# Kernel optimization log

Measured on AMD Instinct MI355X. Metric: run time of the kernel, lower is better.

Reference implementation:

```python
import jax, jax.numpy as jnp
import numpy as np

B, MN, GN, ME, GE = 1, 40962, 65160, 327660, 163848
MEMB = EEMB = 256
H1, H2 = 512, 64
EPS = 1e-5


def setup_inputs() -> dict:
    key = jax.random.key(0)
    ks = jax.random.split(key, 16)
    s = 0.05
    return {
        "gx": jax.random.normal(ks[0], (B, GN, MEMB), jnp.float32),
        "mx": jax.random.normal(ks[1], (B, MN, MEMB), jnp.float32),
        "me_i": jax.random.randint(ks[2], (2, ME), 0, MN),
        "me_x": jax.random.normal(ks[3], (B, ME, EEMB), jnp.float32),
        "g2me_i": jax.random.randint(ks[4], (2, GE), 0, MN),
        "g2me_x": jax.random.normal(ks[5], (B, GE, EEMB), jnp.float32),
        "m2ge_i": jax.random.randint(ks[6], (2, GE), 0, MN),
        "m2ge_x": jax.random.normal(ks[7], (B, GE, EEMB), jnp.float32),
        # learned params (Linear stored as [in, out]; y = x @ W + b, math-equivalent to torch)
        "W1": jax.random.normal(ks[8], (2 * MEMB + EEMB, H1), jnp.float32) * s,
        "b1": jnp.zeros((H1,), jnp.float32),
        "W2": jax.random.normal(ks[9], (H1, H2), jnp.float32) * s,
        "b2": jnp.zeros((H2,), jnp.float32),
        "W3": jax.random.normal(ks[10], (H2, EEMB), jnp.float32) * s,
        "b3": jnp.zeros((EEMB,), jnp.float32),
        # LayerNorm([m_enum, eemb]) -> elementwise affine over last two dims
        "ln_w": jnp.ones((ME, EEMB), jnp.float32),
        "ln_b": jnp.zeros((ME, EEMB), jnp.float32),
    }


def reference(gx, mx, me_i, me_x, g2me_i, g2me_x, m2ge_i, m2ge_x,
              W1, b1, W2, b2, W3, b3, ln_w, ln_b):
    row, col = me_i[0], me_i[1]
    # gather sender/receiver mesh-node features per edge: [B, ME, 2*MEMB+EEMB]
    h = jnp.concatenate([mx[:, row], mx[:, col], me_x], axis=-1)
    h = jax.nn.silu(h @ W1 + b1)
    h = jax.nn.silu(h @ W2 + b2)
    h = h @ W3 + b3
    # LayerNorm over the last TWO dims (m_enum, eemb), as nn.LayerNorm([m_enum, eemb])
    mean = jnp.mean(h, axis=(-2, -1), keepdims=True)
    var = jnp.var(h, axis=(-2, -1), keepdims=True)
    h = (h - mean) * jax.lax.rsqrt(var + EPS) * ln_w + ln_b
    me_x_new = me_x + h
    return (gx, mx, me_i, me_x_new, g2me_i, g2me_x, m2ge_i, m2ge_x)
```

## Files before the change

kernel.cpp:

```cpp
#include <hip/hip_runtime.h>
#include <hip/hip_bf16.h>

typedef unsigned short u16;
typedef unsigned int u32;
typedef __attribute__((ext_vector_type(8))) short bfrag8;
typedef __attribute__((ext_vector_type(4))) float f32x4;

#define ME_N 327660
#define MN_N 40962
#define MEMB_N 256
#define H1_N 512
#define H2_N 64
#define EEMB_N 256
#define LN_EPS 1e-5f
#define NBLK 5120

static __device__ __forceinline__ u16 f2bf(float f) {
  __hip_bfloat16 h = __float2bfloat16(f);
  return *reinterpret_cast<u16*>(&h);
}
static __device__ __forceinline__ float bf2f(u16 u) {
  union { u32 i; float f; } x; x.i = ((u32)u) << 16; return x.f;
}
static __device__ __forceinline__ u32 pack2(float a, float b) {
  return (u32)f2bf(a) | ((u32)f2bf(b) << 16);
}
static __device__ __forceinline__ float silu_f(float x) {
  return x / (1.0f + __expf(-x));
}
static __device__ __forceinline__ void gload_lds16(const void* g, void* l) {
  __builtin_amdgcn_global_load_lds(
      (const __attribute__((address_space(1))) void*)g,
      (__attribute__((address_space(3))) void*)l, 16, 0, 0);
}

__global__ void i2f_kernel(const int* __restrict__ src, float* __restrict__ dst, int n) {
  int i = blockIdx.x * 256 + threadIdx.x;
  if (i < n) dst[i] = (float)src[i];
}

__global__ void bfconv_kernel(const float* __restrict__ src, u16* __restrict__ dst, int n) {
  int i = (blockIdx.x * 256 + threadIdx.x) * 8;
  if (i >= n) return;
  float4 v0 = reinterpret_cast<const float4*>(src + i)[0];
  float4 v1 = reinterpret_cast<const float4*>(src + i)[1];
  uint4 q;
  q.x = pack2(v0.x, v0.y); q.y = pack2(v0.z, v0.w);
  q.z = pack2(v1.x, v1.y); q.w = pack2(v1.z, v1.w);
  *reinterpret_cast<uint4*>(dst + i) = q;
}

__global__ void wconv1_kernel(const float* __restrict__ src, u16* __restrict__ dst) {
  int i = blockIdx.x * 256 + threadIdx.x;
  if (i >= 512 * 768) return;
  int e   = i & 7;
  int l16 = (i >> 3) & 15;
  int k4  = (i >> 7) & 3;
  int ks  = (i >> 9) & 1;
  int rest = i >> 10;
  int kc = rest % 12;
  int J  = rest / 12;
  int n = J * 16 + l16;
  int k = kc * 64 + ks * 32 + k4 * 8 + e;
  dst[i] = f2bf(src[(size_t)k * 512 + n]);
}

__global__ void wconv_kernel(const float* __restrict__ src, u16* __restrict__ dst,
                             int K, int N) {
  int i = blockIdx.x * 256 + threadIdx.x;
  if (i >= K * N) return;
  int n = i / K;
  int k = i - n * K;
  dst[i] = f2bf(src[(size_t)k * N + n]);
}

__launch_bounds__(1024, 4)
__global__ void gemm_fused_kernel(const u16* __restrict__ mxb, const int* __restrict__ me_i,
                                  const float* __restrict__ me_x,
                                  const u16* __restrict__ w1f, const float* __restrict__ b1,
                                  const u16* __restrict__ w2t, const float* __restrict__ b2,
                                  const u16* __restrict__ w3t, const float* __restrict__ b3,
                                  u16* __restrict__ h3, float* __restrict__ partials) {
  __shared__ u16 S[16384];
  __shared__ float red[32];

  const int t = threadIdx.x;
  const int m0 = blockIdx.x * 64;
  const int lane = t & 63;
  const int w = t >> 6;
  const int l16 = lane & 15;
  const int k4 = lane >> 4;
  const int h7 = l16 & 7;

  const int r_st = (t >> 3) & 63;
  const int g_st = t & 7;
  const int gsw = (g_st ^ (r_st & 7)) * 8;
  const int mg = min(m0 + r_st, ME_N - 1);
  const u16* rowr = mxb + (size_t)me_i[mg] * MEMB_N;
  const u16* rowc = mxb + (size_t)me_i[ME_N + mg] * MEMB_N;

  const int r4 = t >> 4;
  const int sub = t & 15;
  const int sgrp = sub >> 1, shalf = sub & 1;
  const int mg4 = min(m0 + r4, ME_N - 1);
  const float* pef = me_x + (size_t)mg4 * EEMB_N + ((sgrp ^ (r4 & 7)) * 8 + shalf * 4);
  const int doff = r4 * 64 + sgrp * 8 + shalf * 4;

  const f32x4 zero = {0.f, 0.f, 0.f, 0.f};
  f32x4 acc[2][4];
#pragma unroll
  for (int jj = 0; jj < 2; ++jj)
#pragma unroll
    for (int i = 0; i < 4; ++i) acc[jj][i] = zero;

  auto stage_dma = [&](int kcn) {
    if (w < 8) {
      const u16* src = (kcn < 4 ? rowr : rowc) + (kcn & 3) * 64 + gsw;
      gload_lds16(src, S + (kcn & 3) * 4096 + w * 512);
    }
  };
  auto loadB = [&](int kc, bfrag8 (&bfr)[2][2]) {
    const u16* wbase = w1f + (size_t)(w * 2) * 12288 + (size_t)kc * 1024 + k4 * 128 + l16 * 8;
#pragma unroll
    for (int ks = 0; ks < 2; ++ks)
#pragma unroll
      for (int jj = 0; jj < 2; ++jj)
        bfr[ks][jj] = *reinterpret_cast<const bfrag8*>(wbase + (size_t)jj * 12288 + ks * 512);
  };
  auto compute = [&](int kc, const bfrag8 (&bfr)[2][2]) {
    const u16* ab = S + (kc & 3) * 4096;
#pragma unroll
    for (int ks = 0; ks < 2; ++ks) {
      bfrag8 a[4];
#pragma unroll
      for (int i = 0; i < 4; ++i)
        a[i] = *reinterpret_cast<const bfrag8*>(
            &ab[(i * 16 + l16) * 64 + (((ks * 4 + k4) ^ h7) * 8)]);
#pragma unroll
      for (int jj = 0; jj < 2; ++jj)
#pragma unroll
        for (int i = 0; i < 4; ++i)
          acc[jj][i] = __builtin_amdgcn_mfma_f32_16x16x32_bf16(bfr[ks][jj], a[i], acc[jj][i], 0, 0, 0);
    }
  };
  auto packA = [&](const float4& fq, int slot) {
    uint2 pq = make_uint2(pack2(fq.x, fq.y), pack2(fq.z, fq.w));
    *reinterpret_cast<uint2*>(S + slot * 4096 + doff) = pq;
  };

#define WAITDMA() if (w < 8) { asm volatile("s_waitcnt vmcnt(10)" ::: "memory"); }
#define BAR() __builtin_amdgcn_s_barrier(); asm volatile("" ::: "memory")
#define LGKM0() asm volatile("s_waitcnt lgkmcnt(0)" ::: "memory")

  bfrag8 B0[2][2], B1[2][2];
  float4 fqA, fqB, fqC, fqD;

  stage_dma(0);
  asm volatile("s_waitcnt vmcnt(63)" ::: "memory");
  stage_dma(1);
  asm volatile("s_waitcnt vmcnt(63)" ::: "memory");
  stage_dma(2);
  loadB(0, B0);

  loadB(1, B1); WAITDMA(); BAR(); stage_dma(3); compute(0, B0);
  loadB(2, B0); WAITDMA(); BAR(); stage_dma(4); compute(1, B1);
  loadB(3, B1); WAITDMA(); BAR(); stage_dma(5); compute(2, B0);
  loadB(4, B0); WAITDMA(); BAR(); stage_dma(6); compute(3, B1);
  loadB(5, B1); WAITDMA(); BAR(); stage_dma(7); compute(4, B0);
  loadB(6, B0); WAITDMA(); BAR();
  fqA = *reinterpret_cast<const float4*>(pef);
  compute(5, B1);
  loadB(7, B1); WAITDMA(); BAR();
  fqB = *reinterpret_cast<const float4*>(pef + 64);
  compute(6, B0);
  loadB(8, B0); WAITDMA(); BAR();
  fqC = *reinterpret_cast<const float4*>(pef + 128);
  compute(7, B1);
  packA(fqA, 0); LGKM0();
  loadB(9, B1); BAR();
  fqD = *reinterpret_cast<const float4*>(pef + 192);
  compute(8, B0);
  packA(fqB, 1); LGKM0();
  loadB(10, B0); BAR();
  compute(9, B1);
  packA(fqC, 2); LGKM0();
  loadB(11, B1); BAR();
  compute(10, B0);
  packA(fqD, 3); LGKM0();
  BAR();
  compute(11, B1);

#undef WAITDMA
#undef BAR
#undef LGKM0

  __syncthreads();

  const int kh = w >> 3;
  const int n2s = w & 3;
  const int ihalf = (w >> 2) & 1;
  const int n2 = n2s * 16 + l16;

  f32x4 acc2p[2];
#pragma unroll
  for (int ii = 0; ii < 2; ++ii) acc2p[ii] = zero;

#pragma unroll
  for (int h = 0; h < 2; ++h) {
    if (kh == h) {
#pragma unroll
      for (int jj = 0; jj < 2; ++jj) {
        const int colbase = (w & 7) * 32 + jj * 16 + k4 * 4;
        const float4 bq = *reinterpret_cast<const float4*>(b1 + h * 256 + colbase);
        const int grp = colbase >> 3, off = colbase & 7;
#pragma unroll
        for (int i = 0; i < 4; ++i) {
          float x0 = silu_f(acc[jj][i][0] + bq.x);
          float x1 = silu_f(acc[jj][i][1] + bq.y);
          float x2 = silu_f(acc[jj][i][2] + bq.z);
          float x3 = silu_f(acc[jj][i][3] + bq.w);
          uint2 pq = make_uint2(pack2(x0, x1), pack2(x2, x3));
          *reinterpret_cast<uint2*>(&S[(i * 16 + l16) * 256 + ((grp ^ h7) * 8 + off)]) = pq;
        }
      }
    }
    __syncthreads();
    if (kh == h) {
#pragma unroll
      for (int ksl = 0; ksl < 8; ++ksl) {
        bfrag8 w2f = *reinterpret_cast<const bfrag8*>(
            w2t + (size_t)n2 * 512 + h * 256 + ksl * 32 + k4 * 8);
#pragma unroll
        for (int ii = 0; ii < 2; ++ii) {
          const int i = ihalf * 2 + ii;
          bfrag8 a2 = *reinterpret_cast<const bfrag8*>(
              &S[(i * 16 + l16) * 256 + (((ksl * 4 + k4) ^ h7) * 8)]);
          acc2p[ii] = __builtin_amdgcn_mfma_f32_16x16x32_bf16(w2f, a2, acc2p[ii], 0, 0, 0);
        }
      }
    }
    __syncthreads();
  }

  float* LDSf = reinterpret_cast<float*>(S);
  u16* h2T = S + 12288;
  if (kh == 1) {
#pragma unroll
    for (int ii = 0; ii < 2; ++ii)
      *reinterpret_cast<f32x4*>(
          &LDSf[(((n2s * 2 + ihalf) * 2 + ii) * 64 + lane) * 4]) = acc2p[ii];
  }
  __syncthreads();
  if (kh == 0) {
    const float4 b2q = *reinterpret_cast<const float4*>(b2 + n2s * 16 + k4 * 4);
    const int grpn = n2s * 2 + (k4 >> 1), offn = (k4 & 1) * 4;
#pragma unroll
    for (int ii = 0; ii < 2; ++ii) {
      const int i = ihalf * 2 + ii;
      f32x4 o = *reinterpret_cast<f32x4*>(
          &LDSf[(((n2s * 2 + ihalf) * 2 + ii) * 64 + lane) * 4]);
      float x0 = silu_f(acc2p[ii][0] + o[0] + b2q.x);
      float x1 = silu_f(acc2p[ii][1] + o[1] + b2q.y);
      float x2 = silu_f(acc2p[ii][2] + o[2] + b2q.z);
      float x3 = silu_f(acc2p[ii][3] + o[3] + b2q.w);
      uint2 pq = make_uint2(pack2(x0, x1), pack2(x2, x3));
      *reinterpret_cast<uint2*>(&h2T[(i * 16 + l16) * 64 + ((grpn ^ h7) * 8 + offn)]) = pq;
    }
  }
  __syncthreads();

  bfrag8 a3[2][4];
#pragma unroll
  for (int ks = 0; ks < 2; ++ks)
#pragma unroll
    for (int i = 0; i < 4; ++i)
      a3[ks][i] = *reinterpret_cast<const bfrag8*>(
          &h2T[(i * 16 + l16) * 64 + (((ks * 4 + k4) ^ h7) * 8)]);
  bfrag8 w3f[2];
#pragma unroll
  for (int ks = 0; ks < 2; ++ks)
    w3f[ks] = *reinterpret_cast<const bfrag8*>(
        w3t + (size_t)(w * 16 + l16) * 64 + ks * 32 + k4 * 8);
  __syncthreads();

  f32x4 acc3[4];
#pragma unroll
  for (int i = 0; i < 4; ++i) acc3[i] = zero;
#pragma unroll
  for (int ks = 0; ks < 2; ++ks)
#pragma unroll
    for (int i = 0; i < 4; ++i)
      acc3[i] = __builtin_amdgcn_mfma_f32_16x16x32_bf16(w3f[ks], a3[ks][i], acc3[i], 0, 0, 0);

  float lsum = 0.f, lsq = 0.f;
  {
    const float4 b3q = *reinterpret_cast<const float4*>(b3 + w * 16 + k4 * 4);
    const int grp3 = w * 2 + (k4 >> 1), off3 = (k4 & 1) * 4;
#pragma unroll
    for (int i = 0; i < 4; ++i) {
      float x0 = acc3[i][0] + b3q.x;
      float x1 = acc3[i][1] + b3q.y;
      float x2 = acc3[i][2] + b3q.z;
      float x3 = acc3[i][3] + b3q.w;
      if (m0 + i * 16 + l16 < ME_N) {
        lsum += (x0 + x1) + (x2 + x3);
        lsq += x0 * x0 + x1 * x1 + x2 * x2 + x3 * x3;
      }
      uint2 pq = make_uint2(pack2(x0, x1), pack2(x2, x3));
      *reinterpret_cast<uint2*>(&S[(i * 16 + l16) * 256 + ((grp3 ^ h7) * 8 + off3)]) = pq;
    }
  }
#pragma unroll
  for (int o = 32; o > 0; o >>= 1) {
    lsum += __shfl_down(lsum, o, 64);
    lsq  += __shfl_down(lsq, o, 64);
  }
  if (lane == 0) { red[w] = lsum; red[16 + w] = lsq; }
  __syncthreads();

  {
    u16* dst = h3 + (size_t)(m0 + r4) * EEMB_N;
#pragma unroll
    for (int q = 0; q < 2; ++q) {
      const int G = sub * 2 + q;
      uint4 v = *reinterpret_cast<const uint4*>(&S[r4 * 256 + ((G ^ (r4 & 7)) * 8)]);
      *reinterpret_cast<uint4*>(dst + G * 8) = v;
    }
  }
  if (t == 0) {
    float s1 = 0.f, s2 = 0.f;
#pragma unroll
    for (int q = 0; q < 16; ++q) { s1 += red[q]; s2 += red[16 + q]; }
    partials[2 * blockIdx.x] = s1;
    partials[2 * blockIdx.x + 1] = s2;
  }
}

__global__ void reduce_kernel(const float* __restrict__ partials, int n,
                              float* __restrict__ stats) {
  __shared__ float s1[256], s2[256];
  float a = 0.f, b = 0.f;
  for (int i = threadIdx.x; i < n; i += 256) { a += partials[2 * i]; b += partials[2 * i + 1]; }
  s1[threadIdx.x] = a; s2[threadIdx.x] = b;
  __syncthreads();
  for (int off = 128; off > 0; off >>= 1) {
    if ((int)threadIdx.x < off) {
      s1[threadIdx.x] += s1[threadIdx.x + off];
      s2[threadIdx.x] += s2[threadIdx.x + off];
    }
    __syncthreads();
  }
  if (threadIdx.x == 0) {
    double cnt = (double)ME_N * (double)EEMB_N;
    double mean = (double)s1[0] / cnt;
    double var = (double)s2[0] / cnt - mean * mean;
    stats[0] = (float)mean;
    stats[1] = (float)(1.0 / sqrt(var + (double)LN_EPS));
  }
}

__launch_bounds__(256)
__global__ void final_kernel(const u16* __restrict__ h3, const float* __restrict__ me_x,
                             const float* __restrict__ ln_w, const float* __restrict__ ln_b,
                             const float* __restrict__ stats, float* __restrict__ out) {
  const size_t total = (size_t)ME_N * EEMB_N;
  size_t i = ((size_t)blockIdx.x * 256 + threadIdx.x) * 8;
  if (i >= total) return;
  const float mean = stats[0], inv = stats[1];
  uint4 hv = *reinterpret_cast<const uint4*>(h3 + i);
  float h[8];
  h[0] = bf2f((u16)(hv.x & 0xffff)); h[1] = bf2f((u16)(hv.x >> 16));
  h[2] = bf2f((u16)(hv.y & 0xffff)); h[3] = bf2f((u16)(hv.y >> 16));
  h[4] = bf2f((u16)(hv.z & 0xffff)); h[5] = bf2f((u16)(hv.z >> 16));
  h[6] = bf2f((u16)(hv.w & 0xffff)); h[7] = bf2f((u16)(hv.w >> 16));
  float4 m0 = reinterpret_cast<const float4*>(me_x + i)[0];
  float4 m1 = reinterpret_cast<const float4*>(me_x + i)[1];
  float4 w0 = reinterpret_cast<const float4*>(ln_w + i)[0];
  float4 w1 = reinterpret_cast<const float4*>(ln_w + i)[1];
  float4 c0 = reinterpret_cast<const float4*>(ln_b + i)[0];
  float4 c1 = reinterpret_cast<const float4*>(ln_b + i)[1];
  float4 o0, o1;
  o0.x = m0.x + (h[0] - mean) * inv * w0.x + c0.x;
  o0.y = m0.y + (h[1] - mean) * inv * w0.y + c0.y;
  o0.z = m0.z + (h[2] - mean) * inv * w0.z + c0.z;
  o0.w = m0.w + (h[3] - mean) * inv * w0.w + c0.w;
  o1.x = m1.x + (h[4] - mean) * inv * w1.x + c1.x;
  o1.y = m1.y + (h[5] - mean) * inv * w1.y + c1.y;
  o1.z = m1.z + (h[6] - mean) * inv * w1.z + c1.z;
  o1.w = m1.w + (h[7] - mean) * inv * w1.w + c1.w;
  reinterpret_cast<float4*>(out + i)[0] = o0;
  reinterpret_cast<float4*>(out + i)[1] = o1;
}

extern "C" void kernel_launch(void* const* d_in, const int* in_sizes, int n_in,
                              void* d_out, int out_size, void* d_ws, size_t ws_size,
                              hipStream_t stream) {
  const float* mx   = (const float*)d_in[1];
  const int*   me_i = (const int*)d_in[2];
  const float* me_x = (const float*)d_in[3];
  const float* W1 = (const float*)d_in[8];
  const float* b1 = (const float*)d_in[9];
  const float* W2 = (const float*)d_in[10];
  const float* b2 = (const float*)d_in[11];
  const float* W3 = (const float*)d_in[12];
  const float* b3 = (const float*)d_in[13];
  const float* ln_w = (const float*)d_in[14];
  const float* ln_b = (const float*)d_in[15];

  char* ws = (char*)d_ws;
  u16* w1f = (u16*)(ws + 0);
  u16* w2t = (u16*)(ws + 786432);
  u16* w3t = (u16*)(ws + 851968);
  u16* mxb = (u16*)(ws + 884736);
  u16* h3  = (u16*)(ws + 21857280);
  float* partials = (float*)(ws + 189629440);
  float* stats    = (float*)(ws + 189670400);

  size_t off[8]; size_t a = 0;
  for (int i = 0; i < 8; ++i) { off[i] = a; a += (size_t)in_sizes[i]; }

  for (int i = 0; i < 8; ++i) {
    if (i == 3) continue;
    if (i == 2 || i == 4 || i == 6) {
      int n = in_sizes[i];
      i2f_kernel<<<(n + 255) / 256, 256, 0, stream>>>(
          (const int*)d_in[i], (float*)d_out + off[i], n);
    } else {
      hipMemcpyAsync((char*)d_out + off[i] * 4, d_in[i], (size_t)in_sizes[i] * 4,
                     hipMemcpyDeviceToDevice, stream);
    }
  }

  wconv1_kernel<<<(512 * 768 + 255) / 256, 256, 0, stream>>>(W1, w1f);
  wconv_kernel<<<(512 * 64 + 255) / 256, 256, 0, stream>>>(W2, w2t, 512, 64);
  wconv_kernel<<<(64 * 256 + 255) / 256, 256, 0, stream>>>(W3, w3t, 64, 256);
  {
    int n = MN_N * MEMB_N;
    bfconv_kernel<<<(n / 8 + 255) / 256, 256, 0, stream>>>(mx, mxb, n);
  }

  gemm_fused_kernel<<<NBLK, 1024, 0, stream>>>(mxb, me_i, me_x, w1f, b1, w2t, b2,
                                               w3t, b3, h3, partials);
  reduce_kernel<<<1, 256, 0, stream>>>(partials, NBLK, stats);

  const size_t total8 = (size_t)ME_N * EEMB_N / 8;
  final_kernel<<<(int)((total8 + 255) / 256), 256, 0, stream>>>(
      h3, me_x, ln_w, ln_b, stats, (float*)d_out + off[3]);
}
```

Measured before the change: 1.011 ms.

## Double the edge tile to 128 rows and DMA fp32 edge features into LDS

The fused MLP kernel now processes 128 edges per block instead of 64, so each W1/W2/W3 fragment loaded from global memory feeds twice as many MFMAs. The me_x edge features are now brought into LDS with async global-to-LDS DMA in fp32 and converted to bf16 at MFMA operand time, replacing the register load and pack step. The vmcnt waits are rebalanced for the new DMA schedule. LDS grows to 128KB and accumulator registers double, which limits occupancy to one block per CU and raises register pressure.

```diff
diff --git a/kernel.cpp b/kernel.cpp
--- a/kernel.cpp
+++ b/kernel.cpp
@@ -13,7 +13,7 @@
 #define H2_N 64
 #define EEMB_N 256
 #define LN_EPS 1e-5f
-#define NBLK 5120
+#define NBLK 2560
 
 static __device__ __forceinline__ u16 f2bf(float f) {
   __hip_bfloat16 h = __float2bfloat16(f);
@@ -81,43 +81,44 @@
                                   const u16* __restrict__ w2t, const float* __restrict__ b2,
                                   const u16* __restrict__ w3t, const float* __restrict__ b3,
                                   u16* __restrict__ h3, float* __restrict__ partials) {
-  __shared__ u16 S[16384];
+  __shared__ u16 S[65536];
   __shared__ float red[32];
 
   const int t = threadIdx.x;
-  const int m0 = blockIdx.x * 64;
+  const int m0 = blockIdx.x * 128;
   const int lane = t & 63;
   const int w = t >> 6;
   const int l16 = lane & 15;
   const int k4 = lane >> 4;
   const int h7 = l16 & 7;
 
-  const int r_st = (t >> 3) & 63;
-  const int g_st = t & 7;
+  const int r_st = t >> 3, g_st = t & 7;
   const int gsw = (g_st ^ (r_st & 7)) * 8;
   const int mg = min(m0 + r_st, ME_N - 1);
   const u16* rowr = mxb + (size_t)me_i[mg] * MEMB_N;
   const u16* rowc = mxb + (size_t)me_i[ME_N + mg] * MEMB_N;
 
-  const int r4 = t >> 4;
-  const int sub = t & 15;
-  const int sgrp = sub >> 1, shalf = sub & 1;
-  const int mg4 = min(m0 + r4, ME_N - 1);
-  const float* pef = me_x + (size_t)mg4 * EEMB_N + ((sgrp ^ (r4 & 7)) * 8 + shalf * 4);
-  const int doff = r4 * 64 + sgrp * 8 + shalf * 4;
+  const int rf0 = t >> 4, g16 = t & 15;
+  const int sgf = (g16 ^ (rf0 & 7)) * 4;
+  const float* pf0 = me_x + (size_t)min(m0 + rf0, ME_N - 1) * EEMB_N + sgf;
+  const float* pf1 = me_x + (size_t)min(m0 + 64 + rf0, ME_N - 1) * EEMB_N + sgf;
 
   const f32x4 zero = {0.f, 0.f, 0.f, 0.f};
-  f32x4 acc[2][4];
+  f32x4 acc[2][8];
 #pragma unroll
   for (int jj = 0; jj < 2; ++jj)
 #pragma unroll
-    for (int i = 0; i < 4; ++i) acc[jj][i] = zero;
-
-  auto stage_dma = [&](int kcn) {
-    if (w < 8) {
-      const u16* src = (kcn < 4 ? rowr : rowc) + (kcn & 3) * 64 + gsw;
-      gload_lds16(src, S + (kcn & 3) * 4096 + w * 512);
-    }
+    for (int i = 0; i < 8; ++i) acc[jj][i] = zero;
+
+  auto stageA = [&](int kcn) {
+    const u16* src = (kcn < 4 ? rowr : rowc) + (kcn & 3) * 64 + gsw;
+    gload_lds16(src, S + (kcn & 3) * 8192 + w * 512);
+  };
+  auto stageF = [&](int kcn) {
+    const int koff = (kcn - 8) * 64;
+    u16* dst = S + 32768 + (kcn & 1) * 16384 + w * 512;
+    gload_lds16(pf0 + koff, dst);
+    gload_lds16(pf1 + koff, dst + 8192);
   };
   auto loadB = [&](int kc, bfrag8 (&bfr)[2][2]) {
     const u16* wbase = w1f + (size_t)(w * 2) * 12288 + (size_t)kc * 1024 + k4 * 128 + l16 * 8;
@@ -127,72 +128,62 @@
       for (int jj = 0; jj < 2; ++jj)
         bfr[ks][jj] = *reinterpret_cast<const bfrag8*>(wbase + (size_t)jj * 12288 + ks * 512);
   };
-  auto compute = [&](int kc, const bfrag8 (&bfr)[2][2]) {
-    const u16* ab = S + (kc & 3) * 4096;
-#pragma unroll
-    for (int ks = 0; ks < 2; ++ks) {
-      bfrag8 a[4];
-#pragma unroll
-      for (int i = 0; i < 4; ++i)
-        a[i] = *reinterpret_cast<const bfrag8*>(
+  auto computeB = [&](int kc, const bfrag8 (&bfr)[2][2]) {
+    const u16* ab = S + (kc & 3) * 8192;
+#pragma unroll
+    for (int ks = 0; ks < 2; ++ks)
+#pragma unroll
+      for (int i = 0; i < 8; ++i) {
+        bfrag8 a = *reinterpret_cast<const bfrag8*>(
             &ab[(i * 16 + l16) * 64 + (((ks * 4 + k4) ^ h7) * 8)]);
 #pragma unroll
-      for (int jj = 0; jj < 2; ++jj)
-#pragma unroll
-        for (int i = 0; i < 4; ++i)
-          acc[jj][i] = __builtin_amdgcn_mfma_f32_16x16x32_bf16(bfr[ks][jj], a[i], acc[jj][i], 0, 0, 0);
-    }
+        for (int jj = 0; jj < 2; ++jj)
+          acc[jj][i] = __builtin_amdgcn_mfma_f32_16x16x32_bf16(bfr[ks][jj], a, acc[jj][i], 0, 0, 0);
+      }
   };
-  auto packA = [&](const float4& fq, int slot) {
-    uint2 pq = make_uint2(pack2(fq.x, fq.y), pack2(fq.z, fq.w));
-    *reinterpret_cast<uint2*>(S + slot * 4096 + doff) = pq;
+  auto computeF = [&](int kc, const bfrag8 (&bfr)[2][2]) {
+    const float* af = reinterpret_cast<const float*>(S + 32768 + (kc & 1) * 16384);
+#pragma unroll
+    for (int ks = 0; ks < 2; ++ks)
+#pragma unroll
+      for (int i = 0; i < 8; ++i) {
+        const int R = i * 16 + l16;
+        f32x4 lo = *reinterpret_cast<const f32x4*>(&af[R * 64 + (ks * 8 + ((k4 * 2) ^ h7)) * 4]);
+        f32x4 hi = *reinterpret_cast<const f32x4*>(&af[R * 64 + (ks * 8 + ((k4 * 2 + 1) ^ h7)) * 4]);
+        union { u32 u[4]; bfrag8 v; } cv;
+        cv.u[0] = pack2(lo[0], lo[1]); cv.u[1] = pack2(lo[2], lo[3]);
+        cv.u[2] = pack2(hi[0], hi[1]); cv.u[3] = pack2(hi[2], hi[3]);
+#pragma unroll
+        for (int jj = 0; jj < 2; ++jj)
+          acc[jj][i] = __builtin_amdgcn_mfma_f32_16x16x32_bf16(bfr[ks][jj], cv.v, acc[jj][i], 0, 0, 0);
+      }
   };
 
-#define WAITDMA() if (w < 8) { asm volatile("s_waitcnt vmcnt(10)" ::: "memory"); }
+#define CB() asm volatile("" ::: "memory")
+#define VW(n) asm volatile("s_waitcnt vmcnt(" #n ")" ::: "memory")
 #define BAR() __builtin_amdgcn_s_barrier(); asm volatile("" ::: "memory")
-#define LGKM0() asm volatile("s_waitcnt lgkmcnt(0)" ::: "memory")
 
   bfrag8 B0[2][2], B1[2][2];
-  float4 fqA, fqB, fqC, fqD;
-
-  stage_dma(0);
-  asm volatile("s_waitcnt vmcnt(63)" ::: "memory");
-  stage_dma(1);
-  asm volatile("s_waitcnt vmcnt(63)" ::: "memory");
-  stage_dma(2);
+
+  stageA(0); CB(); stageA(1); CB(); stageA(2); CB();
   loadB(0, B0);
 
-  loadB(1, B1); WAITDMA(); BAR(); stage_dma(3); compute(0, B0);
-  loadB(2, B0); WAITDMA(); BAR(); stage_dma(4); compute(1, B1);
-  loadB(3, B1); WAITDMA(); BAR(); stage_dma(5); compute(2, B0);
-  loadB(4, B0); WAITDMA(); BAR(); stage_dma(6); compute(3, B1);
-  loadB(5, B1); WAITDMA(); BAR(); stage_dma(7); compute(4, B0);
-  loadB(6, B0); WAITDMA(); BAR();
-  fqA = *reinterpret_cast<const float4*>(pef);
-  compute(5, B1);
-  loadB(7, B1); WAITDMA(); BAR();
-  fqB = *reinterpret_cast<const float4*>(pef + 64);
-  compute(6, B0);
-  loadB(8, B0); WAITDMA(); BAR();
-  fqC = *reinterpret_cast<const float4*>(pef + 128);
-  compute(7, B1);
-  packA(fqA, 0); LGKM0();
-  loadB(9, B1); BAR();
-  fqD = *reinterpret_cast<const float4*>(pef + 192);
-  compute(8, B0);
-  packA(fqB, 1); LGKM0();
-  loadB(10, B0); BAR();
-  compute(9, B1);
-  packA(fqC, 2); LGKM0();
-  loadB(11, B1); BAR();
-  compute(10, B0);
-  packA(fqD, 3); LGKM0();
-  BAR();
-  compute(11, B1);
-
-#undef WAITDMA
+  CB(); loadB(1, B1);  VW(10); BAR(); stageA(3);  computeB(0, B0);
+  CB(); loadB(2, B0);  VW(14); BAR(); stageA(4);  computeB(1, B1);
+  CB(); loadB(3, B1);  VW(18); BAR(); stageA(5);  computeB(2, B0);
+  CB(); loadB(4, B0);  VW(14); BAR(); stageA(6);  computeB(3, B1);
+  CB(); loadB(5, B1);  VW(14); BAR(); stageA(7);  computeB(4, B0);
+  CB(); loadB(6, B0);  VW(14); BAR(); stageF(8);  computeB(5, B1);
+  CB(); loadB(7, B1);  VW(15); BAR(); stageF(9);  computeB(6, B0);
+  CB(); loadB(8, B0);  VW(16); BAR();             computeB(7, B1);
+  CB(); loadB(9, B1);  VW(14); BAR();             computeF(8, B0);
+  CB(); loadB(10, B0); VW(12); BAR(); stageF(10); computeF(9, B1);
+  CB(); loadB(11, B1); VW(4);  BAR(); stageF(11); computeF(10, B0);
+  CB();                VW(0);  BAR();             computeF(11, B1);
+
+#undef CB
+#undef VW
 #undef BAR
-#undef LGKM0
 
   __syncthreads();
 
@@ -201,9 +192,9 @@
   const int ihalf = (w >> 2) & 1;
   const int n2 = n2s * 16 + l16;
 
-  f32x4 acc2p[2];
-#pragma unroll
-  for (int ii = 0; ii < 2; ++ii) acc2p[ii] = zero;
+  f32x4 acc2p[4];
+#pragma unroll
+  for (int ii = 0; ii < 4; ++ii) acc2p[ii] = zero;
 
 #pragma unroll
   for (int h = 0; h < 2; ++h) {
@@ -214,7 +205,7 @@
         const float4 bq = *reinterpret_cast<const float4*>(b1 + h * 256 + colbase);
         const int grp = colbase >> 3, off = colbase & 7;
 #pragma unroll
-        for (int i = 0; i < 4; ++i) {
+        for (int i = 0; i < 8; ++i) {
           float x0 = silu_f(acc[jj][i][0] + bq.x);
           float x1 = silu_f(acc[jj][i][1] + bq.y);
           float x2 = silu_f(acc[jj][i][2] + bq.z);
@@ -231,8 +222,8 @@
         bfrag8 w2f = *reinterpret_cast<const bfrag8*>(
             w2t + (size_t)n2 * 512 + h * 256 + ksl * 32 + k4 * 8);
 #pragma unroll
-        for (int ii = 0; ii < 2; ++ii) {
-          const int i = ihalf * 2 + ii;
+        for (int ii = 0; ii < 4; ++ii) {
+          const int i = ihalf * 4 + ii;
           bfrag8 a2 = *reinterpret_cast<const bfrag8*>(
               &S[(i * 16 + l16) * 256 + (((ksl * 4 + k4) ^ h7) * 8)]);
           acc2p[ii] = __builtin_amdgcn_mfma_f32_16x16x32_bf16(w2f, a2, acc2p[ii], 0, 0, 0);
@@ -242,23 +233,23 @@
     __syncthreads();
   }
 
-  float* LDSf = reinterpret_cast<float*>(S);
-  u16* h2T = S + 12288;
+  float* LDSf = reinterpret_cast<float*>(S + 32768);
+  u16* h2T = S + 49152;
   if (kh == 1) {
 #pragma unroll
-    for (int ii = 0; ii < 2; ++ii)
+    for (int ii = 0; ii < 4; ++ii)
       *reinterpret_cast<f32x4*>(
-          &LDSf[(((n2s * 2 + ihalf) * 2 + ii) * 64 + lane) * 4]) = acc2p[ii];
+          &LDSf[(((n2s * 2 + ihalf) * 4 + ii) * 64 + lane) * 4]) = acc2p[ii];
   }
   __syncthreads();
   if (kh == 0) {
     const float4 b2q = *reinterpret_cast<const float4*>(b2 + n2s * 16 + k4 * 4);
     const int grpn = n2s * 2 + (k4 >> 1), offn = (k4 & 1) * 4;
 #pragma unroll
-    for (int ii = 0; ii < 2; ++ii) {
-      const int i = ihalf * 2 + ii;
+    for (int ii = 0; ii < 4; ++ii) {
+      const int i = ihalf * 4 + ii;
       f32x4 o = *reinterpret_cast<f32x4*>(
-          &LDSf[(((n2s * 2 + ihalf) * 2 + ii) * 64 + lane) * 4]);
+          &LDSf[(((n2s * 2 + ihalf) * 4 + ii) * 64 + lane) * 4]);
       float x0 = silu_f(acc2p[ii][0] + o[0] + b2q.x);
       float x1 = silu_f(acc2p[ii][1] + o[1] + b2q.y);
       float x2 = silu_f(acc2p[ii][2] + o[2] + b2q.z);
@@ -269,11 +260,11 @@
   }
   __syncthreads();
 
-  bfrag8 a3[2][4];
+  bfrag8 a3[2][8];
 #pragma unroll
   for (int ks = 0; ks < 2; ++ks)
 #pragma unroll
-    for (int i = 0; i < 4; ++i)
+    for (int i = 0; i < 8; ++i)
       a3[ks][i] = *reinterpret_cast<const bfrag8*>(
           &h2T[(i * 16 + l16) * 64 + (((ks * 4 + k4) ^ h7) * 8)]);
   bfrag8 w3f[2];
@@ -283,13 +274,13 @@
         w3t + (size_t)(w * 16 + l16) * 64 + ks * 32 + k4 * 8);
   __syncthreads();
 
-  f32x4 acc3[4];
-#pragma unroll
-  for (int i = 0; i < 4; ++i) acc3[i] = zero;
+  f32x4 acc3[8];
+#pragma unroll
+  for (int i = 0; i < 8; ++i) acc3[i] = zero;
 #pragma unroll
   for (int ks = 0; ks < 2; ++ks)
 #pragma unroll
-    for (int i = 0; i < 4; ++i)
+    for (int i = 0; i < 8; ++i)
       acc3[i] = __builtin_amdgcn_mfma_f32_16x16x32_bf16(w3f[ks], a3[ks][i], acc3[i], 0, 0, 0);
 
   float lsum = 0.f, lsq = 0.f;
@@ -297,7 +288,7 @@
     const float4 b3q = *reinterpret_cast<const float4*>(b3 + w * 16 + k4 * 4);
     const int grp3 = w * 2 + (k4 >> 1), off3 = (k4 & 1) * 4;
 #pragma unroll
-    for (int i = 0; i < 4; ++i) {
+    for (int i = 0; i < 8; ++i) {
       float x0 = acc3[i][0] + b3q.x;
       float x1 = acc3[i][1] + b3q.y;
       float x2 = acc3[i][2] + b3q.z;
@@ -319,11 +310,11 @@
   __syncthreads();
 
   {
-    u16* dst = h3 + (size_t)(m0 + r4) * EEMB_N;
-#pragma unroll
-    for (int q = 0; q < 2; ++q) {
-      const int G = sub * 2 + q;
-      uint4 v = *reinterpret_cast<const uint4*>(&S[r4 * 256 + ((G ^ (r4 & 7)) * 8)]);
+    u16* dst = h3 + (size_t)(m0 + r_st) * EEMB_N;
+#pragma unroll
+    for (int q = 0; q < 4; ++q) {
+      const int G = q * 8 + g_st;
+      uint4 v = *reinterpret_cast<const uint4*>(&S[r_st * 256 + ((G ^ (r_st & 7)) * 8)]);
       *reinterpret_cast<uint4*>(dst + G * 8) = v;
     }
   }
```

Measured after the change: 1.018 ms. Within noise of the previous version (+0.7%).
